# Performance work log

Measured on AMD Instinct MI355X. Metric: run time of the kernel, lower is better.

The kernel has to match this reference:

```python
import jax, jax.numpy as jnp
import numpy as np

EMBED_DIM = 1024
NUM_HEADS = 16
HEAD_DIM = EMBED_DIM // NUM_HEADS
SCALING = HEAD_DIM ** -0.5
T, B = 1024, 4


def setup_inputs() -> dict:
    key = jax.random.key(0)
    k1, k2, k3, k4 = jax.random.split(key, 4)
    x_TBC = jax.random.normal(k1, (T, B, EMBED_DIM), dtype=jnp.float32)
    key_padding_mask = jnp.zeros((B, T), dtype=bool)
    edge_bias = jax.random.normal(k2, (B, NUM_HEADS, T, T), dtype=jnp.float32)
    # xavier_uniform-ish init for weights
    lim_qkv = (6.0 / (EMBED_DIM + 3 * EMBED_DIM)) ** 0.5 / (2 ** 0.5)
    w_qkv = jax.random.uniform(k3, (3 * EMBED_DIM, EMBED_DIM), minval=-lim_qkv, maxval=lim_qkv, dtype=jnp.float32)
    b_qkv = jnp.zeros((3 * EMBED_DIM,), dtype=jnp.float32)
    lim_p = (6.0 / (2 * EMBED_DIM)) ** 0.5
    w_proj = jax.random.uniform(k4, (EMBED_DIM, EMBED_DIM), minval=-lim_p, maxval=lim_p, dtype=jnp.float32)
    b_proj = jnp.zeros((EMBED_DIM,), dtype=jnp.float32)
    return {"x_TBC": x_TBC, "key_padding_mask": key_padding_mask, "edge_bias": edge_bias,
            "w_qkv": w_qkv, "b_qkv": b_qkv, "w_proj": w_proj, "b_proj": b_proj}


def reference(x_TBC, key_padding_mask, edge_bias, w_qkv, b_qkv, w_proj, b_proj):
    Tn, Bn, C = x_TBC.shape
    H, Dh = NUM_HEADS, HEAD_DIM
    qkv = x_TBC @ w_qkv.T + b_qkv               # [T,B,3C]
    q, k, v = jnp.split(qkv, 3, axis=-1)
    def split_heads(t):  # [T,B,C] -> [B,H,T,Dh]
        return t.reshape(Tn, Bn, H, Dh).transpose(1, 2, 0, 3)
    q = split_heads(q) * SCALING
    k = split_heads(k)
    v = split_heads(v)
    logits = jnp.einsum('bhtd,bhsd->bhts', q, k) + edge_bias  # [B,H,T,T]
    neg_inf = jnp.finfo(logits.dtype).min
    logits = jnp.where(key_padding_mask[:, None, None, :], neg_inf, logits)
    attn = jax.nn.softmax(logits, axis=-1)
    out = jnp.einsum('bhts,bhsd->bhtd', attn, v)  # [B,H,T,Dh]
    out = out.transpose(2, 0, 1, 3).reshape(Tn, Bn, C)  # [T,B,C]
    out = out @ w_proj.T + b_proj
    return out
```

## Files before the change

### kernel.cpp

```cpp
#include <hip/hip_runtime.h>
#include <stdint.h>
#include <math.h>

#define TT  1024
#define BBN 4
#define CCH 1024
#define HHN 16
#define DHD 64
#define MMR 4096
#define N3  3072

typedef __attribute__((ext_vector_type(4))) float  f32x4;
typedef __attribute__((ext_vector_type(8))) short  s16x8;
typedef __attribute__((ext_vector_type(8))) __bf16 bf16x8;

static __device__ __forceinline__ f32x4 mfma16(s16x8 a, s16x8 b, f32x4 c) {
  return __builtin_amdgcn_mfma_f32_16x16x32_bf16(
      __builtin_bit_cast(bf16x8, a), __builtin_bit_cast(bf16x8, b), c, 0, 0, 0);
}

static __device__ __forceinline__ unsigned short f2bf(float f) {
  union { float f; unsigned int u; } v; v.f = f;
  unsigned int u = v.u;
  return (unsigned short)((u + 0x7FFFu + ((u >> 16) & 1u)) >> 16);
}

typedef const __attribute__((address_space(1))) void GVoid;
typedef __attribute__((address_space(3))) void LVoid;
static __device__ __forceinline__ void gll16(const void* g, void* l) {
  __builtin_amdgcn_global_load_lds((GVoid*)g, (LVoid*)l, 16, 0, 0);
}

#if __has_builtin(__builtin_amdgcn_exp2f)
#define EXP2F(x) __builtin_amdgcn_exp2f(x)
#else
#define EXP2F(x) exp2f(x)
#endif

__global__ void cvt_all(const float* __restrict__ x, const float* __restrict__ wqkv,
                        const float* __restrict__ wproj, unsigned short* __restrict__ out) {
  int i = blockIdx.x * blockDim.x + threadIdx.x;
  const float4* src;
  int off;
  if (i < 1048576)      { src = (const float4*)x;     off = 0; }
  else if (i < 1835008) { src = (const float4*)wqkv;  off = 1048576; }
  else                  { src = (const float4*)wproj; off = 1835008; }
  float4 f = src[i - off];
  ushort4 o;
  o.x = f2bf(f.x); o.y = f2bf(f.y); o.z = f2bf(f.z); o.w = f2bf(f.w);
  ((ushort4*)out)[i] = o;
}

template <int MODE>
__global__ __launch_bounds__(256, 2) void gemm_bt(
    const unsigned short* __restrict__ A, const unsigned short* __restrict__ Bw,
    const float* __restrict__ bias, float* __restrict__ Cout,
    unsigned short* __restrict__ qb, unsigned short* __restrict__ kb,
    unsigned short* __restrict__ vtb, int M, int N, int K) {
  __shared__ __align__(16) unsigned short sA[128 * 64];
  __shared__ __align__(16) unsigned short sB[128 * 64];
  const int tid = threadIdx.x;
  const int l = tid & 63, w = tid >> 6;
  const int g = l >> 4, c = l & 15;
  const int wr = w >> 1, wc = w & 1;
  const int total = gridDim.x * gridDim.y;
  const int flat = blockIdx.y * gridDim.x + blockIdx.x;
  const int wg = (flat & 7) * (total >> 3) + (flat >> 3);
  const int bxs = wg % gridDim.x, bys = wg / gridDim.x;
  const int bm = bys * 128, bn = bxs * 128;
  const int srow = tid >> 3, sch = tid & 7;

  const unsigned short* Agp = A + (size_t)(bm + srow) * K + sch * 8;
  const unsigned short* Bgp = Bw + (size_t)(bn + srow) * K + sch * 8;
  unsigned short* sAw = &sA[w * 512];
  unsigned short* sBw = &sB[w * 512];

  f32x4 acc[4][4] = {};

  for (int k0 = 0; k0 < K; k0 += 64) {
#pragma unroll
    for (int i = 0; i < 4; ++i) {
      gll16(Agp + (size_t)i * 32 * K + k0, sAw + i * 2048);
      gll16(Bgp + (size_t)i * 32 * K + k0, sBw + i * 2048);
    }
    __syncthreads();
#pragma unroll
    for (int kk2 = 0; kk2 < 2; ++kk2) {
      s16x8 af[4], bfr[4];
#pragma unroll
      for (int mi = 0; mi < 4; ++mi)
        af[mi] = *(const s16x8*)&sA[(wr * 64 + mi * 16 + c) * 64 + kk2 * 32 + g * 8];
#pragma unroll
      for (int ni = 0; ni < 4; ++ni)
        bfr[ni] = *(const s16x8*)&sB[(wc * 64 + ni * 16 + c) * 64 + kk2 * 32 + g * 8];
#pragma unroll
      for (int mi = 0; mi < 4; ++mi)
#pragma unroll
        for (int ni = 0; ni < 4; ++ni)
          acc[mi][ni] = mfma16(af[mi], bfr[ni], acc[mi][ni]);
    }
    __syncthreads();
  }

#pragma unroll
  for (int mi = 0; mi < 4; ++mi)
#pragma unroll
    for (int ni = 0; ni < 4; ++ni) {
      const int col = bn + wc * 64 + ni * 16 + c;
      const float bsv = bias[col];
      if (MODE == 0) {
#pragma unroll
        for (int j = 0; j < 4; ++j) {
          const int r = bm + wr * 64 + mi * 16 + g * 4 + j;
          Cout[(size_t)r * N + col] = acc[mi][ni][j] + bsv;
        }
      } else {
        const int part = col >> 10;
        const int rem = col & 1023;
        const int h = rem >> 6, d = rem & 63;
        const float qscale = 0.18033688f;
#pragma unroll
        for (int j = 0; j < 4; ++j) {
          const int r = bm + wr * 64 + mi * 16 + g * 4 + j;
          const int t = r >> 2, bb = r & 3;
          const int bh = bb * 16 + h;
          float av = acc[mi][ni][j] + bsv;
          if (part == 0)      qb[((size_t)bh * 1024 + t) * 64 + d] = f2bf(av * qscale);
          else if (part == 1) kb[((size_t)bh * 1024 + t) * 64 + d] = f2bf(av);
          else                vtb[((size_t)bh * 64 + d) * 1024 + t] = f2bf(av);
        }
      }
    }
}

__global__ __launch_bounds__(256, 3) void attn_kernel(
    const unsigned short* __restrict__ qb, const unsigned short* __restrict__ kb,
    const unsigned short* __restrict__ vtb, const float* __restrict__ eb,
    const unsigned char* __restrict__ mask, unsigned short* __restrict__ ob) {
  __shared__ __align__(16) unsigned short sQ[64 * 64];
  __shared__ __align__(16) unsigned short sK[64 * 64];
  __shared__ __align__(16) unsigned short sV[64 * 64];
  __shared__ __align__(16) unsigned short sP[4][16 * 72];
  const int tid = threadIdx.x;
  const int l = tid & 63, w = tid >> 6;
  const int g = l >> 4, c = l & 15;
  const int flat = blockIdx.y * 16 + blockIdx.x;
  const int wg = (flat & 7) * 128 + (flat >> 3);
  const int q0 = (wg & 15) * 64;
  const int bh = wg >> 4;
  const int b = bh >> 4;
  const int srow = tid >> 3, sch = tid & 7;

  const unsigned short* qg = qb + (size_t)bh * 65536;
  const unsigned short* kg = kb + (size_t)bh * 65536;
  const unsigned short* vg = vtb + (size_t)bh * 65536;
  const float* ebg = eb + (size_t)bh * 1048576 + (size_t)(q0 + w * 16 + g * 4) * 1024;

#pragma unroll
  for (int i = 0; i < 2; ++i) {
    int row = i * 32 + srow;
    gll16(qg + (size_t)(q0 + row) * 64 + (sch ^ (row & 7)) * 8, &sQ[i * 2048 + w * 512]);
  }
  __syncthreads();
  s16x8 qf[2];
#pragma unroll
  for (int kk2 = 0; kk2 < 2; ++kk2) {
    int row = w * 16 + c;
    qf[kk2] = *(const s16x8*)&sQ[row * 64 + (((kk2 * 4 + g) ^ (row & 7)) * 8)];
  }

  const float BS = 1.44269504f;
  float ps[4] = {0.f, 0.f, 0.f, 0.f};
  f32x4 po[4] = {};

  for (int s0 = 0; s0 < TT; s0 += 64) {
#pragma unroll
    for (int i = 0; i < 2; ++i) {
      int row = i * 32 + srow;
      gll16(kg + (size_t)(s0 + row) * 64 + (sch ^ (row & 7)) * 8, &sK[i * 2048 + w * 512]);
      gll16(vg + (size_t)row * 1024 + s0 + (sch ^ (row & 7)) * 8, &sV[i * 2048 + w * 512]);
    }
    __syncthreads();

    float bv[4][4];
#pragma unroll
    for (int ni = 0; ni < 4; ++ni)
#pragma unroll
      for (int j = 0; j < 4; ++j)
        bv[ni][j] = ebg[(size_t)j * 1024 + s0 + ni * 16 + c];
    float mkc[4];
#pragma unroll
    for (int ni = 0; ni < 4; ++ni)
      mkc[ni] = mask[b * TT + s0 + ni * 16 + c] ? -1e30f : -8.0f;

    s16x8 kf[4][2];
#pragma unroll
    for (int ni = 0; ni < 4; ++ni)
#pragma unroll
      for (int kk2 = 0; kk2 < 2; ++kk2) {
        int row = ni * 16 + c;
        kf[ni][kk2] = *(const s16x8*)&sK[row * 64 + (((kk2 * 4 + g) ^ (row & 7)) * 8)];
      }
    f32x4 sc[4] = {};
#pragma unroll
    for (int kk2 = 0; kk2 < 2; ++kk2)
#pragma unroll
      for (int ni = 0; ni < 4; ++ni)
        sc[ni] = mfma16(qf[kk2], kf[ni][kk2], sc[ni]);

#pragma unroll
    for (int ni = 0; ni < 4; ++ni)
#pragma unroll
      for (int j = 0; j < 4; ++j) {
        float x = fmaf(bv[ni][j], BS, sc[ni][j]) + mkc[ni];
        float p = EXP2F(x);
        sP[w][(g * 4 + j) * 72 + ni * 16 + c] = f2bf(p);
        ps[j] += p;
      }
    asm volatile("s_waitcnt lgkmcnt(0)" ::: "memory");
    __builtin_amdgcn_sched_barrier(0);

    s16x8 pf[2];
#pragma unroll
    for (int kk2 = 0; kk2 < 2; ++kk2)
      pf[kk2] = *(const s16x8*)&sP[w][c * 72 + kk2 * 32 + g * 8];

    s16x8 vf[4][2];
#pragma unroll
    for (int nd = 0; nd < 4; ++nd)
#pragma unroll
      for (int kk2 = 0; kk2 < 2; ++kk2) {
        int row = nd * 16 + c;
        vf[nd][kk2] = *(const s16x8*)&sV[row * 64 + (((kk2 * 4 + g) ^ (row & 7)) * 8)];
      }
#pragma unroll
    for (int kk2 = 0; kk2 < 2; ++kk2)
#pragma unroll
      for (int nd = 0; nd < 4; ++nd)
        po[nd] = mfma16(pf[kk2], vf[nd][kk2], po[nd]);

    __syncthreads();
  }

#pragma unroll
  for (int j = 0; j < 4; ++j) {
#pragma unroll
    for (int off = 1; off <= 8; off <<= 1)
      ps[j] += __shfl_xor(ps[j], off, 64);
    ps[j] = 1.0f / ps[j];
  }

  const int h = bh & 15;
#pragma unroll
  for (int nd = 0; nd < 4; ++nd)
#pragma unroll
    for (int j = 0; j < 4; ++j) {
      float val = po[nd][j] * ps[j];
      int t = q0 + w * 16 + g * 4 + j;
      ob[((size_t)t * 4 + b) * 1024 + h * 64 + nd * 16 + c] = f2bf(val);
    }
}

extern "C" void kernel_launch(void* const* d_in, const int* in_sizes, int n_in,
                              void* d_out, int out_size, void* d_ws, size_t ws_size,
                              hipStream_t stream) {
  const float* x      = (const float*)d_in[0];
  const unsigned char* mask = (const unsigned char*)d_in[1];
  const float* ebias  = (const float*)d_in[2];
  const float* wqkv   = (const float*)d_in[3];
  const float* bqkv   = (const float*)d_in[4];
  const float* wproj  = (const float*)d_in[5];
  const float* bproj  = (const float*)d_in[6];
  float* out = (float*)d_out;

  char* ws = (char*)d_ws;
  unsigned short* xb    = (unsigned short*)(ws);
  unsigned short* wqkvb = (unsigned short*)(ws + 8388608);
  unsigned short* wpb   = (unsigned short*)(ws + 14680064);
  unsigned short* qbuf  = (unsigned short*)(ws + 16777216);
  unsigned short* kbuf  = (unsigned short*)(ws + 25165824);
  unsigned short* vtbuf = (unsigned short*)(ws + 33554432);
  unsigned short* obuf  = (unsigned short*)(ws + 41943040);

  cvt_all<<<8192, 256, 0, stream>>>(x, wqkv, wproj, xb);

  gemm_bt<1><<<dim3(24, 32), 256, 0, stream>>>(
      xb, wqkvb, bqkv, nullptr, qbuf, kbuf, vtbuf, MMR, N3, 1024);

  attn_kernel<<<dim3(16, 64), 256, 0, stream>>>(
      qbuf, kbuf, vtbuf, ebias, mask, obuf);

  gemm_bt<0><<<dim3(8, 32), 256, 0, stream>>>(
      obuf, wpb, bproj, out, nullptr, nullptr, nullptr, MMR, 1024, 1024);
}
```

Baseline: 160.7 us.

## Double-buffer K/V tiles and prefetch edge bias in attention kernel

The attention kernel now uses two LDS buffers for K and V and a ping-pong loop unrolled by two. The next tile's K/V LDS loads and its edge-bias and mask register loads are issued before the current tile is computed, so global memory latency overlaps with the MFMA and softmax work. It also raises wave priority around the MFMA blocks with s_setprio. The costs are double the K/V LDS footprint and an extra set of bias registers, which may add spilling or reduce occupancy under the three-blocks-per-CU launch bound.

```diff
diff --git a/kernel.cpp b/kernel.cpp
--- a/kernel.cpp
+++ b/kernel.cpp
@@ -138,8 +138,8 @@
     const unsigned short* __restrict__ vtb, const float* __restrict__ eb,
     const unsigned char* __restrict__ mask, unsigned short* __restrict__ ob) {
   __shared__ __align__(16) unsigned short sQ[64 * 64];
-  __shared__ __align__(16) unsigned short sK[64 * 64];
-  __shared__ __align__(16) unsigned short sV[64 * 64];
+  __shared__ __align__(16) unsigned short sK[2][64 * 64];
+  __shared__ __align__(16) unsigned short sV[2][64 * 64];
   __shared__ __align__(16) unsigned short sP[4][16 * 72];
   const int tid = threadIdx.x;
   const int l = tid & 63, w = tid >> 6;
@@ -156,12 +156,95 @@
   const unsigned short* vg = vtb + (size_t)bh * 65536;
   const float* ebg = eb + (size_t)bh * 1048576 + (size_t)(q0 + w * 16 + g * 4) * 1024;
 
+  const float BS = 1.44269504f;
+  float ps[4] = {0.f, 0.f, 0.f, 0.f};
+  f32x4 po[4] = {};
+  float bvA[4][4], bvB[4][4], mkA[4], mkB[4];
+
+#define STAGE_KV(t, p) do {                                                      \
+    int ss_ = (t) * 64;                                                          \
+    _Pragma("unroll")                                                            \
+    for (int i_ = 0; i_ < 2; ++i_) {                                             \
+      int row_ = i_ * 32 + srow;                                                 \
+      gll16(kg + (size_t)(ss_ + row_) * 64 + (sch ^ (row_ & 7)) * 8,             \
+            &sK[p][i_ * 2048 + w * 512]);                                        \
+      gll16(vg + (size_t)row_ * 1024 + ss_ + (sch ^ (row_ & 7)) * 8,             \
+            &sV[p][i_ * 2048 + w * 512]);                                        \
+    } } while (0)
+
+#define LOAD_BIAS(t, bv, mk) do {                                                \
+    int ss_ = (t) * 64;                                                          \
+    _Pragma("unroll")                                                            \
+    for (int ni_ = 0; ni_ < 4; ++ni_) {                                          \
+      _Pragma("unroll")                                                          \
+      for (int j_ = 0; j_ < 4; ++j_)                                             \
+        bv[ni_][j_] = ebg[(size_t)j_ * 1024 + ss_ + ni_ * 16 + c];               \
+      mk[ni_] = mask[b * TT + ss_ + ni_ * 16 + c] ? -1e30f : -8.0f;              \
+    } } while (0)
+
+#define COMPUTE(p, bv, mk) do {                                                  \
+                                                                  \
+    s16x8 kf_[4][2];                                                             \
+    _Pragma("unroll")                                                            \
+    for (int ni_ = 0; ni_ < 4; ++ni_)                                            \
+      _Pragma("unroll")                                                          \
+      for (int k2_ = 0; k2_ < 2; ++k2_) {                                        \
+        int row_ = ni_ * 16 + c;                                                 \
+        kf_[ni_][k2_] = *(const s16x8*)&sK[p][row_ * 64 +                        \
+                         (((k2_ * 4 + g) ^ (row_ & 7)) * 8)];                    \
+      }                                                                          \
+    f32x4 sc_[4] = {};                                                           \
+    __builtin_amdgcn_s_setprio(1);                                               \
+    _Pragma("unroll")                                                            \
+    for (int k2_ = 0; k2_ < 2; ++k2_)                                            \
+      _Pragma("unroll")                                                          \
+      for (int ni_ = 0; ni_ < 4; ++ni_)                                          \
+        sc_[ni_] = mfma16(qf[k2_], kf_[ni_][k2_], sc_[ni_]);                     \
+    __builtin_amdgcn_s_setprio(0);                                               \
+                 \
+    _Pragma("unroll")                                                            \
+    for (int ni_ = 0; ni_ < 4; ++ni_)                                            \
+      _Pragma("unroll")                                                          \
+      for (int j_ = 0; j_ < 4; ++j_) {                                           \
+        float x_ = fmaf(bv[ni_][j_], BS, sc_[ni_][j_]) + mk[ni_];                \
+        float p_ = EXP2F(x_);                                                    \
+        sP[w][(g * 4 + j_) * 72 + ni_ * 16 + c] = f2bf(p_);                      \
+        ps[j_] += p_;                                                            \
+      }                                                                          \
+                  \
+    s16x8 vf_[4][2];                                                             \
+    _Pragma("unroll")                                                            \
+    for (int nd_ = 0; nd_ < 4; ++nd_)                                            \
+      _Pragma("unroll")                                                          \
+      for (int k2_ = 0; k2_ < 2; ++k2_) {                                        \
+        int row_ = nd_ * 16 + c;                                                 \
+        vf_[nd_][k2_] = *(const s16x8*)&sV[p][row_ * 64 +                        \
+                         (((k2_ * 4 + g) ^ (row_ & 7)) * 8)];                    \
+      }                                                                          \
+    asm volatile("s_waitcnt lgkmcnt(0)" ::: "memory");                           \
+    __builtin_amdgcn_sched_barrier(0);                                           \
+    s16x8 pf_[2];                                                                \
+    _Pragma("unroll")                                                            \
+    for (int k2_ = 0; k2_ < 2; ++k2_)                                            \
+      pf_[k2_] = *(const s16x8*)&sP[w][c * 72 + k2_ * 32 + g * 8];               \
+    __builtin_amdgcn_s_setprio(1);                                               \
+    _Pragma("unroll")                                                            \
+    for (int k2_ = 0; k2_ < 2; ++k2_)                                            \
+      _Pragma("unroll")                                                          \
+      for (int nd_ = 0; nd_ < 4; ++nd_)                                          \
+        po[nd_] = mfma16(pf_[k2_], vf_[nd_][k2_], po[nd_]);                      \
+    __builtin_amdgcn_s_setprio(0);                                               \
+  } while (0)
+
 #pragma unroll
   for (int i = 0; i < 2; ++i) {
     int row = i * 32 + srow;
     gll16(qg + (size_t)(q0 + row) * 64 + (sch ^ (row & 7)) * 8, &sQ[i * 2048 + w * 512]);
   }
+  STAGE_KV(0, 0);
+  LOAD_BIAS(0, bvA, mkA);
   __syncthreads();
+
   s16x8 qf[2];
 #pragma unroll
   for (int kk2 = 0; kk2 < 2; ++kk2) {
@@ -169,78 +252,27 @@
     qf[kk2] = *(const s16x8*)&sQ[row * 64 + (((kk2 * 4 + g) ^ (row & 7)) * 8)];
   }
 
-  const float BS = 1.44269504f;
-  float ps[4] = {0.f, 0.f, 0.f, 0.f};
-  f32x4 po[4] = {};
-
-  for (int s0 = 0; s0 < TT; s0 += 64) {
-#pragma unroll
-    for (int i = 0; i < 2; ++i) {
-      int row = i * 32 + srow;
-      gll16(kg + (size_t)(s0 + row) * 64 + (sch ^ (row & 7)) * 8, &sK[i * 2048 + w * 512]);
-      gll16(vg + (size_t)row * 1024 + s0 + (sch ^ (row & 7)) * 8, &sV[i * 2048 + w * 512]);
-    }
+  STAGE_KV(1, 1);
+  LOAD_BIAS(1, bvB, mkB);
+  COMPUTE(0, bvA, mkA);
+  for (int it = 1; it < 8; ++it) {
     __syncthreads();
-
-    float bv[4][4];
-#pragma unroll
-    for (int ni = 0; ni < 4; ++ni)
-#pragma unroll
-      for (int j = 0; j < 4; ++j)
-        bv[ni][j] = ebg[(size_t)j * 1024 + s0 + ni * 16 + c];
-    float mkc[4];
-#pragma unroll
-    for (int ni = 0; ni < 4; ++ni)
-      mkc[ni] = mask[b * TT + s0 + ni * 16 + c] ? -1e30f : -8.0f;
-
-    s16x8 kf[4][2];
-#pragma unroll
-    for (int ni = 0; ni < 4; ++ni)
-#pragma unroll
-      for (int kk2 = 0; kk2 < 2; ++kk2) {
-        int row = ni * 16 + c;
-        kf[ni][kk2] = *(const s16x8*)&sK[row * 64 + (((kk2 * 4 + g) ^ (row & 7)) * 8)];
-      }
-    f32x4 sc[4] = {};
-#pragma unroll
-    for (int kk2 = 0; kk2 < 2; ++kk2)
-#pragma unroll
-      for (int ni = 0; ni < 4; ++ni)
-        sc[ni] = mfma16(qf[kk2], kf[ni][kk2], sc[ni]);
-
-#pragma unroll
-    for (int ni = 0; ni < 4; ++ni)
-#pragma unroll
-      for (int j = 0; j < 4; ++j) {
-        float x = fmaf(bv[ni][j], BS, sc[ni][j]) + mkc[ni];
-        float p = EXP2F(x);
-        sP[w][(g * 4 + j) * 72 + ni * 16 + c] = f2bf(p);
-        ps[j] += p;
-      }
-    asm volatile("s_waitcnt lgkmcnt(0)" ::: "memory");
-    __builtin_amdgcn_sched_barrier(0);
-
-    s16x8 pf[2];
-#pragma unroll
-    for (int kk2 = 0; kk2 < 2; ++kk2)
-      pf[kk2] = *(const s16x8*)&sP[w][c * 72 + kk2 * 32 + g * 8];
-
-    s16x8 vf[4][2];
-#pragma unroll
-    for (int nd = 0; nd < 4; ++nd)
-#pragma unroll
-      for (int kk2 = 0; kk2 < 2; ++kk2) {
-        int row = nd * 16 + c;
-        vf[nd][kk2] = *(const s16x8*)&sV[row * 64 + (((kk2 * 4 + g) ^ (row & 7)) * 8)];
-      }
-#pragma unroll
-    for (int kk2 = 0; kk2 < 2; ++kk2)
-#pragma unroll
-      for (int nd = 0; nd < 4; ++nd)
-        po[nd] = mfma16(pf[kk2], vf[nd][kk2], po[nd]);
-
+    STAGE_KV(2 * it, 0);
+    LOAD_BIAS(2 * it, bvA, mkA);
+    COMPUTE(1, bvB, mkB);
     __syncthreads();
-  }
+    if (2 * it + 1 < 16) {
+      STAGE_KV(2 * it + 1, 1);
+      LOAD_BIAS(2 * it + 1, bvB, mkB);
+    }
+    COMPUTE(0, bvA, mkA);
+  }
+  __syncthreads();
+  COMPUTE(1, bvB, mkB);
+
+#undef STAGE_KV
+#undef LOAD_BIAS
+#undef COMPUTE
 
 #pragma unroll
   for (int j = 0; j < 4; ++j) {
```

New measurement: 164.0 us. 2.1% more time.
